# Kernel optimization log

Measured on AMD Instinct MI355X. Metric: run time of the kernel, lower is better.

Reference implementation:

```python
import jax, jax.numpy as jnp
import numpy as np

THRESH = 1.0   # kwargs_spikes['thresh']
VRESET = 0.0   # kwargs_spikes['vreset'] (not None -> hard reset branch)

@jax.custom_vjp
def rectangle_spike(x):
    # Rectangle surrogate-gradient spike fn: forward heaviside
    return (x >= 0.0).astype(x.dtype)

def _rs_fwd(x):
    return rectangle_spike(x), x

def _rs_bwd(x, g):
    # rectangular surrogate: grad passes where |u - thresh| < 0.5
    return (g * (jnp.abs(x) < 0.5).astype(g.dtype),)

rectangle_spike.defvjp(_rs_fwd, _rs_bwd)

def conv2d(x, w, b):
    # NCHW same-padding conv (padding = kernel_size // 2 with k=3 == SAME)
    y = jax.lax.conv_general_dilated(x, w, (1, 1), 'SAME',
                                     dimension_numbers=('NCHW', 'OIHW', 'NCHW'))
    return y + b[None, :, None, None]

def setup_inputs() -> dict:
    key = jax.random.key(0)
    ks = jax.random.split(key, 4)
    B, T, Cin, H, W = 8, 5, 64, 64, 64
    Cout, K = 64, 3
    # event-frame style sparse binary input
    events = (jax.random.uniform(ks[0], (B, T, Cin, H, W)) < 0.3).astype(jnp.float32)
    scale_in = 1.0 / np.sqrt(Cin * K * K)
    w_in = (jax.random.normal(ks[1], (2 * Cout, Cin, K, K)) * scale_in).astype(jnp.float32)
    b_in = jnp.zeros((2 * Cout,), jnp.float32)
    scale_g = 1.0 / np.sqrt(Cout * K * K)
    w_gate = (jax.random.normal(ks[2], (2 * Cout, Cout, K, K)) * scale_g).astype(jnp.float32)
    b_gate = jnp.zeros((2 * Cout,), jnp.float32)
    thresh_decay = jnp.ones((Cout,), jnp.float32) * 0.9
    return {'events': events, 'w_in': w_in, 'b_in': b_in,
            'w_gate': w_gate, 'b_gate': b_gate, 'thresh_decay': thresh_decay}

def reference(events, w_in, b_in, w_gate, b_gate, thresh_decay):
    # events: [B, T, Cin, H, W] -> [T, B, Cin, H, W], time-reversed (index_select with
    # descending indices, as in the torch forward)
    ev = jnp.flip(jnp.swapaxes(events, 0, 1), axis=0)
    T, B, _, H, W = ev.shape
    Cout = thresh_decay.shape[0]
    vmem0 = jnp.zeros((B, Cout, H, W), ev.dtype)
    spike0 = jnp.zeros((B, Cout, H, W), ev.dtype)

    def step(carry, xs):
        vmem, spike_last = carry
        x, t = xs
        # input path and recurrent gate path each emit 2*Cout channels:
        # first half = current injection, second half = gate pre-activation
        cur_in, gate_in = jnp.split(conv2d(x, w_in, b_in), 2, axis=1)
        cur_g, gate_g = jnp.split(conv2d(spike_last, w_gate, b_gate), 2, axis=1)
        gate = jax.nn.sigmoid(gate_in + gate_g)
        current = cur_in + cur_g
        # per-channel decaying threshold: thresh * thresh_decay^t
        thresh_t = THRESH * thresh_decay[None, :, None, None] ** t
        vmem = gate * vmem + current
        spike = rectangle_spike(vmem - thresh_t)
        # vreset is not None -> hard reset to VRESET where spiked
        vmem = vmem * (1.0 - spike) + VRESET * spike
        return (vmem, spike), spike

    _, spikes = jax.lax.scan(step, (vmem0, spike0),
                             (ev, jnp.arange(T, dtype=ev.dtype)))
    # readout='avg': average firing map over time steps  [B, Cout, H, W]
    return jnp.mean(spikes, axis=0)
```

## Files before the change

kernel.cpp:

```cpp
#include <hip/hip_runtime.h>
#include <cmath>


typedef __attribute__((ext_vector_type(8))) short short8;
typedef __attribute__((ext_vector_type(4))) float floatx4;

#define HW 64
#define TT 5
#define PLANE 4096
#define WP_ELEMS 147456
#define CDIM 136
#define UELEMS (4 * 66 * CDIM)

__device__ __forceinline__ ushort f2bf_rne(float f) {
  uint u = __float_as_uint(f);
  return (ushort)((u + 0x7FFFu + ((u >> 16) & 1u)) >> 16);
}
__device__ __forceinline__ float bf2f(ushort h) {
  return __uint_as_float(((uint)h) << 16);
}

__global__ __launch_bounds__(256) void prep_weights(
    const float* __restrict__ w_in, const float* __restrict__ w_gate,
    ushort* __restrict__ Wp)
{
  int idx = blockIdx.x * 256 + threadIdx.x;
  if (idx >= WP_ELEMS) return;
  int j   = idx & 7;
  int o   = (idx >> 3) & 127;
  int q   = (idx >> 10) & 3;
  int ks  = (idx >> 12) & 3;
  int tap = idx >> 14;
  int c   = ks * 32 + q * 8 + j;
  int g = o >> 4, i = o & 15;
  int row = (i >> 3) * 64 + (g * 8 + (i & 7));
  float w = (c < 64) ? w_in[(row * 64 + c) * 9 + tap]
                     : w_gate[(row * 64 + (c - 64)) * 9 + tap];
  ushort h = f2bf_rne(w);
  float r1 = w - bf2f(h);
  ushort m = f2bf_rne(r1);
  float r2 = r1 - bf2f(m);
  ushort l = f2bf_rne(r2);
  Wp[idx] = h;
  Wp[WP_ELEMS + idx] = m;
  Wp[2 * WP_ELEMS + idx] = l;
}

__global__ __launch_bounds__(1024, 4) void snn_step(
    const float*  __restrict__ events,
    const ushort* __restrict__ Wp,
    const float*  __restrict__ b_in,
    const float*  __restrict__ b_gate,
    const float*  __restrict__ tdec,
    float*        __restrict__ vmem,
    const ushort* __restrict__ s_src,
    ushort*       __restrict__ s_dst,
    float*        __restrict__ outp,
    int t)
{
  __shared__ ushort U[UELEMS];

  const int tid = threadIdx.x;
  const int b   = blockIdx.x >> 5;
  const int br  = blockIdx.x & 31;
  const int r0  = 2 * br;

  const int lane = tid & 63;
  const int g    = (tid >> 6) & 7;
  const int half = tid >> 9;
  const int ln   = lane & 15;
  const int q    = lane >> 4;

  for (int i = tid; i < UELEMS / 8; i += 1024) ((short8*)U)[i] = short8{0,0,0,0,0,0,0,0};
  __syncthreads();

  {
    const int c   = tid & 63;
    const int row = (tid >> 6) & 3;
    const int seg = (tid >> 8) & 3;
    const int r   = r0 + row - 1;
    if (r >= 0 && r < HW) {
      const float* src = events + ((size_t)(b * TT + (TT - 1 - t)) * 64 + c) * PLANE
                         + r * HW + seg * 16;
      float v[16];
#pragma unroll
      for (int k = 0; k < 4; ++k) {
        float4 f = ((const float4*)src)[k];
        v[4*k+0] = f.x; v[4*k+1] = f.y; v[4*k+2] = f.z; v[4*k+3] = f.w;
      }
#pragma unroll
      for (int k = 0; k < 16; ++k)
        U[(row * 66 + 1 + seg * 16 + k) * CDIM + c] = (v[k] != 0.f) ? 0x3F80 : 0;
    }
  }
  {
    const int col   = tid & 63;
    const int row   = (tid >> 6) & 3;
    const int chunk = (tid >> 8) & 3;
    const int r     = r0 + row - 1;
    if (r >= 0 && r < HW) {
      const ushort* src = s_src + ((size_t)((b * HW + r) * HW + col)) * 64 + chunk * 16;
      ushort* dst = U + (row * 66 + col + 1) * CDIM + 64 + chunk * 16;
      *(short8*)(dst)     = *(const short8*)(src);
      *(short8*)(dst + 8) = *(const short8*)(src + 8);
    }
  }
  __syncthreads();

  floatx4 acc[4];
#pragma unroll
  for (int tt = 0; tt < 4; ++tt) acc[tt] = floatx4{0.f, 0.f, 0.f, 0.f};

  const int laneB = ln * CDIM + q * 8;
  const ushort* wpl = Wp + (size_t)q * 1024 + (g * 16 + ln) * 8;

  for (int tap = 0; tap < 9; ++tap) {
    const int kh = tap / 3, kw = tap % 3;
    short8 Ah[4], Am[4], Al[4];
    const ushort* wpt = wpl + tap * 16384;
#pragma unroll
    for (int ks = 0; ks < 4; ++ks) {
      Ah[ks] = *(const short8*)(wpt + ks * 4096);
      Am[ks] = *(const short8*)(wpt + WP_ELEMS + ks * 4096);
      Al[ks] = *(const short8*)(wpt + 2 * WP_ELEMS + ks * 4096);
    }
#pragma unroll
    for (int tt = 0; tt < 4; ++tt) {
      const int xbase = (half + kh) * 66 * CDIM + (tt * 16 + kw) * CDIM;
#pragma unroll
      for (int ks = 0; ks < 4; ++ks) {
        short8 B = *(const short8*)(U + xbase + ks * 32 + laneB);
        acc[tt] = __builtin_amdgcn_mfma_f32_16x16x32_bf16(Ah[ks], B, acc[tt], 0, 0, 0);
        acc[tt] = __builtin_amdgcn_mfma_f32_16x16x32_bf16(Am[ks], B, acc[tt], 0, 0, 0);
        acc[tt] = __builtin_amdgcn_mfma_f32_16x16x32_bf16(Al[ks], B, acc[tt], 0, 0, 0);
      }
    }
  }

  const bool t0 = (t == 0), tL = (t == TT - 1);
  float bc[4], bg[4], th[4];
  {
    const int qe = q & 1;
#pragma unroll
    for (int r = 0; r < 4; ++r) {
      const int co = g * 8 + qe * 4 + r;
      bc[r] = b_in[co] + b_gate[co];
      bg[r] = b_in[64 + co] + b_gate[64 + co];
      th[r] = powf(tdec[co], (float)t);
    }
  }
  const int hh = r0 + half;
#pragma unroll
  for (int tt = 0; tt < 4; ++tt) {
    const int col = tt * 16 + ln;
#pragma unroll
    for (int r = 0; r < 4; ++r) {
      const float other = __shfl_xor(acc[tt][r], 32, 64);
      if (q < 2) {
        const int co = g * 8 + q * 4 + r;
        const size_t idx  = ((size_t)((b * 64 + co) * HW + hh)) * HW + col;
        const size_t sidx = ((size_t)((b * HW + hh) * HW + col)) * 64 + co;
        const float cur  = acc[tt][r] + bc[r];
        const float gp   = other + bg[r];
        const float gate = 1.f / (1.f + expf(-gp));
        const float v    = gate * vmem[idx] + cur;
        const bool fired = (v >= th[r]);
        vmem[idx]  = fired ? 0.f : v;
        s_dst[sidx] = fired ? (ushort)0x3F80 : (ushort)0;
        float o = (t0 ? 0.f : outp[idx]) + (fired ? 1.f : 0.f);
        if (tL) o *= 0.2f;
        outp[idx] = o;
      }
    }
  }
}

extern "C" void kernel_launch(void* const* d_in, const int* in_sizes, int n_in,
                              void* d_out, int out_size, void* d_ws, size_t ws_size,
                              hipStream_t stream) {
  const float* events = (const float*)d_in[0];
  const float* w_in   = (const float*)d_in[1];
  const float* b_in   = (const float*)d_in[2];
  const float* w_gate = (const float*)d_in[3];
  const float* b_gate = (const float*)d_in[4];
  const float* tdec   = (const float*)d_in[5];
  float* out = (float*)d_out;

  char* base = (char*)d_ws;
  float*  vmem = (float*)base;
  ushort* sA   = (ushort*)(base + 8388608);
  ushort* sB   = (ushort*)(base + 12582912);
  ushort* Wp   = (ushort*)(base + 16777216);

  hipMemsetAsync(base, 0, 12582912, stream);

  hipLaunchKernelGGL(prep_weights, dim3(576), dim3(256), 0, stream, w_in, w_gate, Wp);

  for (int t = 0; t < TT; ++t) {
    const ushort* ssrc = (t & 1) ? sB : sA;
    ushort*       sdst = (t & 1) ? sA : sB;
    hipLaunchKernelGGL(snn_step, dim3(256), dim3(1024), 0, stream,
                       events, Wp, b_in, b_gate, tdec, vmem, ssrc, sdst, out, t);
  }
}
```

Baseline: 286.0 us.

## Switch conv MFMA from split-bf16 to multi-limb int8 with binary activations

Replaces the three-way bf16 weight split with a four-limb int8 fixed-point decomposition and uses i8 MFMA (16x16x64). Activations (events and spikes) are stored as int8 0/1, halving LDS and global traffic. Events are pre-converted once into a channel-last int8 layout, and bias and threshold powers are precomputed into a table. This trades more MFMA instructions per K-step for cheaper int8 throughput and smaller data. It relies on the fixed-point weight representation being accurate enough to reproduce the spike decisions.

Measured after the change: 247.3 us. 1.16x faster.

```diff
diff --git a/kernel.cpp b/kernel.cpp
--- a/kernel.cpp
+++ b/kernel.cpp
@@ -2,176 +2,203 @@
 #include <cmath>
 
 
-typedef __attribute__((ext_vector_type(8))) short short8;
-typedef __attribute__((ext_vector_type(4))) float floatx4;
+typedef __attribute__((ext_vector_type(4))) int intx4;
 
 #define HW 64
 #define TT 5
 #define PLANE 4096
-#define WP_ELEMS 147456
-#define CDIM 136
-#define UELEMS (4 * 66 * CDIM)
-
-__device__ __forceinline__ ushort f2bf_rne(float f) {
-  uint u = __float_as_uint(f);
-  return (ushort)((u + 0x7FFFu + ((u >> 16) & 1u)) >> 16);
-}
-__device__ __forceinline__ float bf2f(ushort h) {
-  return __uint_as_float(((uint)h) << 16);
-}
-
-__global__ __launch_bounds__(256) void prep_weights(
+#define CSTR 144
+#define USIZE (4 * 66 * CSTR)
+#define WPL 147456
+
+__global__ __launch_bounds__(256) void prep_w(
     const float* __restrict__ w_in, const float* __restrict__ w_gate,
-    ushort* __restrict__ Wp)
+    const float* __restrict__ b_in, const float* __restrict__ b_gate,
+    const float* __restrict__ tdec,
+    signed char* __restrict__ Wp, float* __restrict__ tabs)
 {
-  int idx = blockIdx.x * 256 + threadIdx.x;
-  if (idx >= WP_ELEMS) return;
-  int j   = idx & 7;
-  int o   = (idx >> 3) & 127;
-  int q   = (idx >> 10) & 3;
-  int ks  = (idx >> 12) & 3;
-  int tap = idx >> 14;
-  int c   = ks * 32 + q * 8 + j;
-  int g = o >> 4, i = o & 15;
-  int row = (i >> 3) * 64 + (g * 8 + (i & 7));
-  float w = (c < 64) ? w_in[(row * 64 + c) * 9 + tap]
-                     : w_gate[(row * 64 + (c - 64)) * 9 + tap];
-  ushort h = f2bf_rne(w);
-  float r1 = w - bf2f(h);
-  ushort m = f2bf_rne(r1);
-  float r2 = r1 - bf2f(m);
-  ushort l = f2bf_rne(r2);
-  Wp[idx] = h;
-  Wp[WP_ELEMS + idx] = m;
-  Wp[2 * WP_ELEMS + idx] = l;
+  const int idx = blockIdx.x * 256 + threadIdx.x;
+  if (idx < 9216) {
+    const int o   = idx & 127;
+    const int q   = (idx >> 7) & 3;
+    const int ks  = (idx >> 9) & 1;
+    const int tap = idx >> 10;
+    const int g = o >> 4, i = o & 15;
+    const int row = (i >> 3) * 64 + g * 8 + (i & 7);
+    int p1[4], p2[4], p3[4], p4[4];
+#pragma unroll
+    for (int wd = 0; wd < 4; ++wd) {
+      int v1 = 0, v2 = 0, v3 = 0, v4 = 0;
+#pragma unroll
+      for (int jb = 0; jb < 4; ++jb) {
+        const int j = wd * 4 + jb;
+        const int c = ks * 64 + q * 16 + j;
+        const float w = (c < 64) ? w_in[(row * 64 + c) * 9 + tap]
+                                 : w_gate[(row * 64 + (c - 64)) * 9 + tap];
+        float a1 = fminf(fmaxf(rintf(w * 256.f), -127.f), 127.f);
+        float r1 = w * 256.f - a1;
+        float a2 = rintf(r1 * 128.f);
+        float r2 = r1 * 128.f - a2;
+        float a3 = rintf(r2 * 128.f);
+        float r3 = r2 * 128.f - a3;
+        float a4 = rintf(r3 * 128.f);
+        v1 |= ((int)a1 & 255) << (8 * jb);
+        v2 |= ((int)a2 & 255) << (8 * jb);
+        v3 |= ((int)a3 & 255) << (8 * jb);
+        v4 |= ((int)a4 & 255) << (8 * jb);
+      }
+      p1[wd] = v1; p2[wd] = v2; p3[wd] = v3; p4[wd] = v4;
+    }
+    intx4* d = (intx4*)(Wp + (size_t)idx * 16);
+    d[0]                          = intx4{p1[0], p1[1], p1[2], p1[3]};
+    *(intx4*)((char*)d + WPL)     = intx4{p2[0], p2[1], p2[2], p2[3]};
+    *(intx4*)((char*)d + 2 * WPL) = intx4{p3[0], p3[1], p3[2], p3[3]};
+    *(intx4*)((char*)d + 3 * WPL) = intx4{p4[0], p4[1], p4[2], p4[3]};
+  }
+  if (idx < 448) {
+    if (idx < 128) tabs[idx] = b_in[idx] + b_gate[idx];
+    else {
+      const int t = (idx - 128) >> 6, co = (idx - 128) & 63;
+      tabs[idx] = powf(tdec[co], (float)t);
+    }
+  }
+}
+
+__global__ __launch_bounds__(256) void prep_ev(
+    const float* __restrict__ ev, signed char* __restrict__ evb)
+{
+  const int row  = blockIdx.x * 4 + (threadIdx.x >> 6);
+  const int w    = threadIdx.x & 63;
+  const int b  = row / (TT * HW);
+  const int rm = row % (TT * HW);
+  const int tp = rm / HW;
+  const int h  = rm % HW;
+  const float* src = ev + ((size_t)(b * TT + tp) * 64) * PLANE + h * HW + w;
+  signed char* dst = evb + ((size_t)((b * TT + tp) * PLANE + h * HW + w)) * 64;
+#pragma unroll
+  for (int k = 0; k < 8; ++k) {
+    unsigned long long pk = 0;
+#pragma unroll
+    for (int j = 0; j < 8; ++j)
+      pk |= (src[(size_t)(k * 8 + j) * PLANE] != 0.f)
+              ? (1ull << (8 * j)) : 0ull;
+    *(unsigned long long*)(dst + k * 8) = pk;
+  }
 }
 
 __global__ __launch_bounds__(1024, 4) void snn_step(
-    const float*  __restrict__ events,
-    const ushort* __restrict__ Wp,
-    const float*  __restrict__ b_in,
-    const float*  __restrict__ b_gate,
-    const float*  __restrict__ tdec,
-    float*        __restrict__ vmem,
-    const ushort* __restrict__ s_src,
-    ushort*       __restrict__ s_dst,
-    float*        __restrict__ outp,
+    const signed char* __restrict__ evb,
+    const signed char* __restrict__ Wp,
+    const float*       __restrict__ tabs,
+    float*             __restrict__ vmem,
+    const signed char* __restrict__ s_src,
+    signed char*       __restrict__ s_dst,
+    float*             __restrict__ outp,
     int t)
 {
-  __shared__ ushort U[UELEMS];
+  __shared__ signed char U[USIZE];
 
   const int tid = threadIdx.x;
   const int b   = blockIdx.x >> 5;
-  const int br  = blockIdx.x & 31;
-  const int r0  = 2 * br;
+  const int r0  = (blockIdx.x & 31) * 2;
 
   const int lane = tid & 63;
   const int g    = (tid >> 6) & 7;
-  const int half = tid >> 9;
+  const int hf   = tid >> 9;
   const int ln   = lane & 15;
   const int q    = lane >> 4;
 
-  for (int i = tid; i < UELEMS / 8; i += 1024) ((short8*)U)[i] = short8{0,0,0,0,0,0,0,0};
+  for (int i = tid; i < USIZE / 16; i += 1024) ((intx4*)U)[i] = intx4{0, 0, 0, 0};
+
+  const int srow = tid >> 8;
+  const int scol = (tid >> 2) & 63;
+  const int sch  = tid & 3;
+  const int sr   = r0 + srow - 1;
+  const bool svalid = (sr >= 0) && (sr < HW);
+  signed char* du = U + (srow * 66 + scol + 1) * CSTR + sch * 32;
+  const signed char* gsrc = nullptr;
+  if (svalid) {
+    gsrc = (sch < 2)
+      ? evb + ((size_t)(b * TT + (TT - 1 - t)) * PLANE + sr * HW + scol) * 64 + sch * 32
+      : s_src + ((size_t)((b * HW + sr) * HW + scol)) * 64 + (sch - 2) * 32;
+  }
   __syncthreads();
-
-  {
-    const int c   = tid & 63;
-    const int row = (tid >> 6) & 3;
-    const int seg = (tid >> 8) & 3;
-    const int r   = r0 + row - 1;
-    if (r >= 0 && r < HW) {
-      const float* src = events + ((size_t)(b * TT + (TT - 1 - t)) * 64 + c) * PLANE
-                         + r * HW + seg * 16;
-      float v[16];
-#pragma unroll
-      for (int k = 0; k < 4; ++k) {
-        float4 f = ((const float4*)src)[k];
-        v[4*k+0] = f.x; v[4*k+1] = f.y; v[4*k+2] = f.z; v[4*k+3] = f.w;
+  if (svalid) {
+    *(intx4*)(du)      = *(const intx4*)(gsrc);
+    *(intx4*)(du + 16) = *(const intx4*)(gsrc + 16);
+  }
+  __syncthreads();
+
+  intx4 acc1[4], acc2[4], acc3[4], acc4[4];
+#pragma unroll
+  for (int tt = 0; tt < 4; ++tt) {
+    acc1[tt] = intx4{0,0,0,0}; acc2[tt] = intx4{0,0,0,0};
+    acc3[tt] = intx4{0,0,0,0}; acc4[tt] = intx4{0,0,0,0};
+  }
+
+  const int laneB = ln * CSTR + q * 16;
+  const signed char* wlane = Wp + q * 2048 + (g * 16 + ln) * 16;
+
+  for (int tap = 0; tap < 9; ++tap) {
+    const int kh = (tap * 11) >> 5;
+    const int kw = tap - 3 * kh;
+#pragma unroll
+    for (int ks = 0; ks < 2; ++ks) {
+      const signed char* wp = wlane + (tap * 2 + ks) * 8192;
+      const intx4 A1 = *(const intx4*)(wp);
+      const intx4 A2 = *(const intx4*)(wp + WPL);
+      const intx4 A3 = *(const intx4*)(wp + 2 * WPL);
+      const intx4 A4 = *(const intx4*)(wp + 3 * WPL);
+      const signed char* ub = U + (hf + kh) * (66 * CSTR) + kw * CSTR + ks * 64 + laneB;
+#pragma unroll
+      for (int tt = 0; tt < 4; ++tt) {
+        const intx4 B = *(const intx4*)(ub + tt * (16 * CSTR));
+        acc1[tt] = __builtin_amdgcn_mfma_i32_16x16x64_i8(A1, B, acc1[tt], 0, 0, 0);
+        acc2[tt] = __builtin_amdgcn_mfma_i32_16x16x64_i8(A2, B, acc2[tt], 0, 0, 0);
+        acc3[tt] = __builtin_amdgcn_mfma_i32_16x16x64_i8(A3, B, acc3[tt], 0, 0, 0);
+        acc4[tt] = __builtin_amdgcn_mfma_i32_16x16x64_i8(A4, B, acc4[tt], 0, 0, 0);
       }
-#pragma unroll
-      for (int k = 0; k < 16; ++k)
-        U[(row * 66 + 1 + seg * 16 + k) * CDIM + c] = (v[k] != 0.f) ? 0x3F80 : 0;
-    }
-  }
-  {
-    const int col   = tid & 63;
-    const int row   = (tid >> 6) & 3;
-    const int chunk = (tid >> 8) & 3;
-    const int r     = r0 + row - 1;
-    if (r >= 0 && r < HW) {
-      const ushort* src = s_src + ((size_t)((b * HW + r) * HW + col)) * 64 + chunk * 16;
-      ushort* dst = U + (row * 66 + col + 1) * CDIM + 64 + chunk * 16;
-      *(short8*)(dst)     = *(const short8*)(src);
-      *(short8*)(dst + 8) = *(const short8*)(src + 8);
-    }
-  }
-  __syncthreads();
-
-  floatx4 acc[4];
-#pragma unroll
-  for (int tt = 0; tt < 4; ++tt) acc[tt] = floatx4{0.f, 0.f, 0.f, 0.f};
-
-  const int laneB = ln * CDIM + q * 8;
-  const ushort* wpl = Wp + (size_t)q * 1024 + (g * 16 + ln) * 8;
-
-  for (int tap = 0; tap < 9; ++tap) {
-    const int kh = tap / 3, kw = tap % 3;
-    short8 Ah[4], Am[4], Al[4];
-    const ushort* wpt = wpl + tap * 16384;
-#pragma unroll
-    for (int ks = 0; ks < 4; ++ks) {
-      Ah[ks] = *(const short8*)(wpt + ks * 4096);
-      Am[ks] = *(const short8*)(wpt + WP_ELEMS + ks * 4096);
-      Al[ks] = *(const short8*)(wpt + 2 * WP_ELEMS + ks * 4096);
-    }
-#pragma unroll
-    for (int tt = 0; tt < 4; ++tt) {
-      const int xbase = (half + kh) * 66 * CDIM + (tt * 16 + kw) * CDIM;
-#pragma unroll
-      for (int ks = 0; ks < 4; ++ks) {
-        short8 B = *(const short8*)(U + xbase + ks * 32 + laneB);
-        acc[tt] = __builtin_amdgcn_mfma_f32_16x16x32_bf16(Ah[ks], B, acc[tt], 0, 0, 0);
-        acc[tt] = __builtin_amdgcn_mfma_f32_16x16x32_bf16(Am[ks], B, acc[tt], 0, 0, 0);
-        acc[tt] = __builtin_amdgcn_mfma_f32_16x16x32_bf16(Al[ks], B, acc[tt], 0, 0, 0);
-      }
     }
   }
 
   const bool t0 = (t == 0), tL = (t == TT - 1);
+  const int co0 = g * 8 + (q & 1) * 4;
   float bc[4], bg[4], th[4];
-  {
-    const int qe = q & 1;
-#pragma unroll
-    for (int r = 0; r < 4; ++r) {
-      const int co = g * 8 + qe * 4 + r;
-      bc[r] = b_in[co] + b_gate[co];
-      bg[r] = b_in[64 + co] + b_gate[64 + co];
-      th[r] = powf(tdec[co], (float)t);
-    }
-  }
-  const int hh = r0 + half;
+#pragma unroll
+  for (int r = 0; r < 4; ++r) {
+    bc[r] = tabs[co0 + r];
+    bg[r] = tabs[64 + co0 + r];
+    th[r] = tabs[128 + t * 64 + co0 + r];
+  }
+  const int hh = r0 + hf;
 #pragma unroll
   for (int tt = 0; tt < 4; ++tt) {
     const int col = tt * 16 + ln;
+    uint fm = 0;
 #pragma unroll
     for (int r = 0; r < 4; ++r) {
-      const float other = __shfl_xor(acc[tt][r], 32, 64);
+      const float mine = fmaf((float)acc1[tt][r], 0x1p-8f,
+                         fmaf((float)acc2[tt][r], 0x1p-15f,
+                         fmaf((float)acc3[tt][r], 0x1p-22f,
+                              (float)acc4[tt][r] * 0x1p-29f)));
+      const float other = __shfl_xor(mine, 32, 64);
       if (q < 2) {
-        const int co = g * 8 + q * 4 + r;
-        const size_t idx  = ((size_t)((b * 64 + co) * HW + hh)) * HW + col;
-        const size_t sidx = ((size_t)((b * HW + hh) * HW + col)) * 64 + co;
-        const float cur  = acc[tt][r] + bc[r];
+        const int co = co0 + r;
+        const size_t idx = ((size_t)((b * 64 + co) * HW + hh)) * HW + col;
+        const float cur  = mine + bc[r];
         const float gp   = other + bg[r];
         const float gate = 1.f / (1.f + expf(-gp));
         const float v    = gate * vmem[idx] + cur;
         const bool fired = (v >= th[r]);
-        vmem[idx]  = fired ? 0.f : v;
-        s_dst[sidx] = fired ? (ushort)0x3F80 : (ushort)0;
+        vmem[idx] = fired ? 0.f : v;
+        fm |= fired ? (1u << (8 * r)) : 0u;
         float o = (t0 ? 0.f : outp[idx]) + (fired ? 1.f : 0.f);
         if (tL) o *= 0.2f;
         outp[idx] = o;
       }
     }
+    if (q < 2)
+      *(uint*)(s_dst + ((size_t)((b * HW + hh) * HW + col)) * 64 + co0) = fm;
   }
 }
 
@@ -187,19 +214,23 @@
   float* out = (float*)d_out;
 
   char* base = (char*)d_ws;
-  float*  vmem = (float*)base;
-  ushort* sA   = (ushort*)(base + 8388608);
-  ushort* sB   = (ushort*)(base + 12582912);
-  ushort* Wp   = (ushort*)(base + 16777216);
-
-  hipMemsetAsync(base, 0, 12582912, stream);
-
-  hipLaunchKernelGGL(prep_weights, dim3(576), dim3(256), 0, stream, w_in, w_gate, Wp);
+  float*       vmem = (float*)base;
+  signed char* sA   = (signed char*)(base + 8388608);
+  signed char* sB   = (signed char*)(base + 10485760);
+  signed char* evb  = (signed char*)(base + 12582912);
+  signed char* Wp   = (signed char*)(base + 23068672);
+  float*       tabs = (float*)(base + 23658496);
+
+  hipMemsetAsync(base, 0, 10485760, stream);
+
+  hipLaunchKernelGGL(prep_w,  dim3(36),  dim3(256), 0, stream,
+                     w_in, w_gate, b_in, b_gate, tdec, Wp, tabs);
+  hipLaunchKernelGGL(prep_ev, dim3(640), dim3(256), 0, stream, events, evb);
 
   for (int t = 0; t < TT; ++t) {
-    const ushort* ssrc = (t & 1) ? sB : sA;
-    ushort*       sdst = (t & 1) ? sA : sB;
+    const signed char* ssrc = (t & 1) ? sB : sA;
+    signed char*       sdst = (t & 1) ? sA : sB;
     hipLaunchKernelGGL(snn_step, dim3(256), dim3(1024), 0, stream,
-                       events, Wp, b_in, b_gate, tdec, vmem, ssrc, sdst, out, t);
-  }
-}
+                       evb, Wp, tabs, vmem, ssrc, sdst, out, t);
+  }
+}
```
